# Performance work log

Measured on AMD Instinct MI355X. Metric: run time of the kernel, lower is better.

## Reference

```python
import jax, jax.numpy as jnp
import numpy as np

N_NODES = 50000
N_EDGES = 600000
CH = 128      # units / channels
RBF = 200     # ceil(cutoff/gap) = ceil(20.0/0.1)
LOG2 = 0.6931471805599453


def shifted_softplus(x):
    # tf.where(x < 14, softplus(where(x < 14, x, 0)), x) - log(2)
    safe = jnp.where(x < 14.0, x, jnp.zeros_like(x))
    return jnp.where(x < 14.0, jax.nn.softplus(safe), x) - LOG2


def _glorot(key, shape):
    fan_in = shape[0] if len(shape) > 1 else shape[0]
    fan_out = shape[-1]
    lim = np.sqrt(6.0 / (fan_in + fan_out))
    return jax.random.uniform(key, shape, jnp.float32, -lim, lim)


def setup_inputs() -> dict:
    key = jax.random.key(0)
    ks = jax.random.split(key, 12)
    rbf = jax.random.uniform(ks[0], (N_EDGES, RBF), jnp.float32)
    x = jax.random.normal(ks[1], (N_NODES, CH), jnp.float32)
    src = jax.random.randint(ks[2], (N_EDGES,), 0, N_NODES, jnp.int32)
    return {
        "rbf": rbf,
        "x": x,
        "src": src,
        "w1": _glorot(ks[3], (RBF, CH)),
        "b1": _glorot(ks[4], (CH,)),
        "w2": _glorot(ks[5], (CH, CH)),
        "b2": _glorot(ks[6], (CH,)),
        "w3": _glorot(ks[7], (CH, CH)),
        "w4": _glorot(ks[8], (CH, CH)),
        "b4": _glorot(ks[9], (CH,)),
        "w5": _glorot(ks[10], (CH, CH)),
        "b5": _glorot(ks[11], (CH,)),
    }


def reference(rbf, x, src, w1, b1, w2, b2, w3, w4, b4, w5, b5):
    # filter-generating MLP on edge RBF features: [E, RBF] -> [E, CH]
    h = shifted_softplus(rbf @ w1 + b1)
    w = shifted_softplus(h @ w2 + b2)
    # node feature transform, gather to edges by SOURCE index
    f = x @ w3                         # [N, CH]
    wf = w * f[src]                    # [E, CH] broadcast_node_to_edges + multiply
    # scatter-sum edges back to SOURCE nodes
    conv = jax.ops.segment_sum(wf, src, num_segments=N_NODES)  # [N, CH]
    # output MLP + residual
    y = shifted_softplus(conv @ w4 + b4)
    v = y @ w5 + b5
    return x + v
```

## Files before the change

kernel.cpp:

```cpp
#include <hip/hip_runtime.h>

#define CH      128
#define RBFD    200
#define NNODES  50000
#define NEDGES  600000
#define LOG2F_  0.6931471805599453f

#define W1F_ELEMS (8 * 7 * 64 * 8)
#define W2F_ELEMS (8 * 4 * 64 * 8)
#define WF_TOT    (W1F_ELEMS + W2F_ELEMS)

typedef __attribute__((ext_vector_type(8))) __bf16 bf16x8;
typedef __attribute__((ext_vector_type(4))) float  f32x4;

__device__ __forceinline__ float ssp(float x) {
    float e  = __expf(x);
    float sp = __logf(1.0f + e);
    sp = (x < 14.0f) ? sp : x;
    return sp - LOG2F_;
}

__device__ __forceinline__ unsigned short f2bf(float f) {
    union { float f; unsigned int u; } v; v.f = f;
    unsigned int r = v.u + 0x7FFFu + ((v.u >> 16) & 1u);
    return (unsigned short)(r >> 16);
}

__device__ __forceinline__ float bf2f(unsigned short s) {
    union { unsigned int u; float f; } v; v.u = ((unsigned int)s) << 16;
    return v.f;
}

__device__ __forceinline__ unsigned short cvt1bf(float f) {
    unsigned int u;
    asm("v_cvt_pk_bf16_f32 %0, %1, %2" : "=v"(u) : "v"(f), "v"(f));
    return (unsigned short)u;
}

__device__ __forceinline__ bf16x8 load_cvt8(const float* p) {
    float4 f0 = *(const float4*)p;
    float4 f1 = *(const float4*)(p + 4);
    union { unsigned int u[4]; bf16x8 v; } r;
    asm("v_cvt_pk_bf16_f32 %0, %1, %2" : "=v"(r.u[0]) : "v"(f0.x), "v"(f0.y));
    asm("v_cvt_pk_bf16_f32 %0, %1, %2" : "=v"(r.u[1]) : "v"(f0.z), "v"(f0.w));
    asm("v_cvt_pk_bf16_f32 %0, %1, %2" : "=v"(r.u[2]) : "v"(f1.x), "v"(f1.y));
    asm("v_cvt_pk_bf16_f32 %0, %1, %2" : "=v"(r.u[3]) : "v"(f1.z), "v"(f1.w));
    return r.v;
}

__global__ __launch_bounds__(256) void prep_weights_frag(const float* __restrict__ w1,
                                                         const float* __restrict__ w2,
                                                         unsigned short* __restrict__ w1F,
                                                         unsigned short* __restrict__ w2F) {
    int i = blockIdx.x * 256 + threadIdx.x;
    if (i < W1F_ELEMS) {
        int frag = i >> 9;
        int lane = (i >> 3) & 63;
        int j    = i & 7;
        int nt = frag / 7, kt = frag % 7;
        int n = nt * 16 + (lane & 15);
        int k = kt * 32 + (lane >> 4) * 8 + j;
        w1F[i] = (k < RBFD) ? f2bf(w1[k * CH + n]) : (unsigned short)0;
    } else if (i < WF_TOT) {
        int q = i - W1F_ELEMS;
        int frag = q >> 9;
        int lane = (q >> 3) & 63;
        int j    = q & 7;
        int nt = frag >> 2, kt = frag & 3;
        int n = nt * 16 + (lane & 15);
        int k = kt * 32 + (lane >> 4) * 8 + j;
        w2F[q] = f2bf(w2[k * CH + n]);
    }
}

__global__ __launch_bounds__(256) void k_hist(const int* __restrict__ src, int* __restrict__ cur) {
    int e = blockIdx.x * 256 + threadIdx.x;
    if (e < NEDGES) atomicAdd(&cur[src[e]], 1);
}

__global__ __launch_bounds__(256) void k_scan1(const int* __restrict__ cur, int* __restrict__ bsum) {
    __shared__ int s[256];
    const int t = threadIdx.x;
    int i = blockIdx.x * 256 + t;
    s[t] = (i < NNODES) ? cur[i] : 0;
    __syncthreads();
    for (int d = 128; d > 0; d >>= 1) {
        if (t < d) s[t] += s[t + d];
        __syncthreads();
    }
    if (t == 0) bsum[blockIdx.x] = s[0];
}

__global__ __launch_bounds__(256) void k_scan2(const int* __restrict__ bsum, int* __restrict__ bpre) {
    __shared__ int s[256];
    const int t = threadIdx.x;
    int v0 = (t < 196) ? bsum[t] : 0;
    s[t] = v0;
    __syncthreads();
    for (int d = 1; d < 256; d <<= 1) {
        int v = (t >= d) ? s[t - d] : 0;
        __syncthreads();
        s[t] += v;
        __syncthreads();
    }
    if (t < 196) bpre[t] = s[t] - v0;
}

__global__ __launch_bounds__(256) void k_scan3(const int* __restrict__ deg_in,
                                               const int* __restrict__ bpre,
                                               int* __restrict__ csr_off,
                                               int* __restrict__ cur) {
    __shared__ int s[256];
    const int t = threadIdx.x, b = blockIdx.x;
    const int i = b * 256 + t;
    int d0 = (i < NNODES) ? deg_in[i] : 0;
    s[t] = d0;
    __syncthreads();
    for (int d = 1; d < 256; d <<= 1) {
        int v = (t >= d) ? s[t - d] : 0;
        __syncthreads();
        s[t] += v;
        __syncthreads();
    }
    if (i < NNODES) {
        int ex = bpre[b] + s[t] - d0;
        csr_off[i] = ex;
        cur[i] = ex;
    }
    if (i == NNODES - 1) csr_off[NNODES] = NEDGES;
}

__global__ __launch_bounds__(256) void k_fill(const int* __restrict__ src,
                                              int* __restrict__ cur,
                                              int* __restrict__ eidx) {
    int e = blockIdx.x * 256 + threadIdx.x;
    if (e < NEDGES) {
        int pos = atomicAdd(&cur[src[e]], 1);
        eidx[pos] = e;
    }
}

__global__ __launch_bounds__(256, 8) void edge_kernel4(const float* __restrict__ rbf,
                                                       const float* __restrict__ b1v,
                                                       const float* __restrict__ b2v,
                                                       const unsigned short* __restrict__ w1F,
                                                       const unsigned short* __restrict__ w2F,
                                                       unsigned short* __restrict__ wbuf) {
    __shared__ unsigned short tile[4][16 * 128];
    const int t = threadIdx.x;
    const int lane = t & 63;
    const int wv = t >> 6;
    const int l15 = lane & 15;
    const int lg  = lane >> 4;
    const size_t erow0 = (size_t)blockIdx.x * 64 + (size_t)wv * 16;
    char* myb = (char*)(tile[wv]);

    const bf16x8* w1v = (const bf16x8*)w1F;
    const bf16x8* w2v = (const bf16x8*)w2F;

    bf16x8 a1[7];
    const float* arow = rbf + (erow0 + l15) * RBFD;
#pragma unroll
    for (int kt = 0; kt < 6; kt++)
        a1[kt] = load_cvt8(arow + kt * 32 + lg * 8);
    if (lg == 0) {
        a1[6] = load_cvt8(arow + 192);
    } else {
        union { unsigned int u[4]; bf16x8 v; } z;
        z.u[0] = z.u[1] = z.u[2] = z.u[3] = 0;
        a1[6] = z.v;
    }

    const int myrow0 = lg * 4;

#pragma unroll
    for (int nt = 0; nt < 8; nt++) {
        f32x4 acc = {0.f, 0.f, 0.f, 0.f};
#pragma unroll
        for (int kt = 0; kt < 7; kt++) {
            bf16x8 b = w1v[((nt * 7 + kt) << 6) + lane];
            acc = __builtin_amdgcn_mfma_f32_16x16x32_bf16(a1[kt], b, acc, 0, 0, 0);
        }
        const float bias = b1v[nt * 16 + l15];
#pragma unroll
        for (int r = 0; r < 4; r++) {
            const int row = myrow0 + r;
            const int colb = (nt * 32 + l15 * 2) ^ ((row & 7) << 4);
            *(unsigned short*)(myb + row * 256 + colb) = cvt1bf(ssp(acc[r] + bias));
        }
    }

    bf16x8 a2[4];
#pragma unroll
    for (int kt = 0; kt < 4; kt++) {
        const int boff = l15 * 256 + ((kt * 64 + lg * 16) ^ ((l15 & 7) << 4));
        a2[kt] = *(const bf16x8*)(myb + boff);
    }

#pragma unroll
    for (int nt = 0; nt < 8; nt++) {
        f32x4 acc = {0.f, 0.f, 0.f, 0.f};
#pragma unroll
        for (int kt = 0; kt < 4; kt++) {
            bf16x8 b = w2v[((nt * 4 + kt) << 6) + lane];
            acc = __builtin_amdgcn_mfma_f32_16x16x32_bf16(a2[kt], b, acc, 0, 0, 0);
        }
        const float bias = b2v[nt * 16 + l15];
#pragma unroll
        for (int r = 0; r < 4; r++) {
            const int row = myrow0 + r;
            const int colb = (nt * 32 + l15 * 2) ^ ((row & 7) << 4);
            *(unsigned short*)(myb + row * 256 + colb) = cvt1bf(ssp(acc[r] + bias));
        }
    }

    {
        const int row = lane >> 2, q = lane & 3;
        float4 o[4];
#pragma unroll
        for (int j = 0; j < 4; j++) {
            const int boff = row * 256 + ((q * 64 + j * 16) ^ ((row & 7) << 4));
            o[j] = *(const float4*)(myb + boff);
        }
        float4* gdst = (float4*)((char*)wbuf + (erow0 + row) * 256 + q * 64);
#pragma unroll
        for (int j = 0; j < 4; j++) gdst[j] = o[j];
    }
}

__global__ __launch_bounds__(256) void node_gather2(const float* __restrict__ x,
                                                    const float* __restrict__ w3,
                                                    const float* __restrict__ w4,
                                                    const float* __restrict__ b4,
                                                    const float* __restrict__ w5,
                                                    const float* __restrict__ b5,
                                                    const unsigned short* __restrict__ wbuf,
                                                    const int* __restrict__ eidx,
                                                    const int* __restrict__ csr_off,
                                                    float* __restrict__ out,
                                                    int n_nodes) {
    __shared__ float A[32 * 128];
    __shared__ float B[32 * 128];
    const int t = threadIdx.x;
    const int n0 = blockIdx.x * 32;
    const int rows = min(32, n_nodes - n0);

    {
        const float4* g = (const float4*)(x + (size_t)n0 * CH);
        float4* s = (float4*)A;
        for (int i = t; i < rows * 32; i += 256) s[i] = g[i];
    }
    __syncthreads();

    const int c = t & 127, eh = t >> 7;
    float acc[16];

#pragma unroll
    for (int i = 0; i < 16; i++) acc[i] = 0.f;
    for (int k = 0; k < 128; k += 4) {
        const float wa = w3[(k + 0) * CH + c];
        const float wb = w3[(k + 1) * CH + c];
        const float wc = w3[(k + 2) * CH + c];
        const float wd = w3[(k + 3) * CH + c];
#pragma unroll
        for (int i = 0; i < 16; i++) {
            const float4 v = *(const float4*)&A[(eh * 16 + i) * CH + k];
            acc[i] = fmaf(v.x, wa, acc[i]);
            acc[i] = fmaf(v.y, wb, acc[i]);
            acc[i] = fmaf(v.z, wc, acc[i]);
            acc[i] = fmaf(v.w, wd, acc[i]);
        }
    }
#pragma unroll
    for (int i = 0; i < 16; i++) B[(eh * 16 + i) * 128 + c] = acc[i];
    __syncthreads();

    {
        const int lane = t & 63, wv = t >> 6;
        const int c0 = lane * 2;
        for (int rr = 0; rr < 8; rr++) {
            const int r = wv * 8 + rr;
            const int n = n0 + r;
            float s0 = 0.f, s1 = 0.f;
            if (n < n_nodes) {
                const int o0 = csr_off[n], o1 = csr_off[n + 1];
                int j = o0;
                for (; j + 3 < o1; j += 4) {
                    const int ea = eidx[j], eb = eidx[j + 1], ec = eidx[j + 2], ed = eidx[j + 3];
                    const unsigned ua = *(const unsigned*)(wbuf + (size_t)ea * CH + c0);
                    const unsigned ub = *(const unsigned*)(wbuf + (size_t)eb * CH + c0);
                    const unsigned uc = *(const unsigned*)(wbuf + (size_t)ec * CH + c0);
                    const unsigned ud = *(const unsigned*)(wbuf + (size_t)ed * CH + c0);
                    s0 += bf2f((unsigned short)ua) + bf2f((unsigned short)ub)
                        + bf2f((unsigned short)uc) + bf2f((unsigned short)ud);
                    s1 += bf2f((unsigned short)(ua >> 16)) + bf2f((unsigned short)(ub >> 16))
                        + bf2f((unsigned short)(uc >> 16)) + bf2f((unsigned short)(ud >> 16));
                }
                for (; j < o1; j++) {
                    const unsigned ua = *(const unsigned*)(wbuf + (size_t)eidx[j] * CH + c0);
                    s0 += bf2f((unsigned short)ua);
                    s1 += bf2f((unsigned short)(ua >> 16));
                }
            }
            const float2 f2 = *(const float2*)&B[r * 128 + c0];
            float2 v2;
            v2.x = (n < n_nodes) ? f2.x * s0 : 0.f;
            v2.y = (n < n_nodes) ? f2.y * s1 : 0.f;
            *(float2*)&B[r * 128 + c0] = v2;
        }
    }
    __syncthreads();

#pragma unroll
    for (int i = 0; i < 16; i++) acc[i] = 0.f;
    for (int k = 0; k < 128; k += 4) {
        const float wa = w4[(k + 0) * CH + c];
        const float wb = w4[(k + 1) * CH + c];
        const float wc = w4[(k + 2) * CH + c];
        const float wd = w4[(k + 3) * CH + c];
#pragma unroll
        for (int i = 0; i < 16; i++) {
            const float4 v = *(const float4*)&B[(eh * 16 + i) * CH + k];
            acc[i] = fmaf(v.x, wa, acc[i]);
            acc[i] = fmaf(v.y, wb, acc[i]);
            acc[i] = fmaf(v.z, wc, acc[i]);
            acc[i] = fmaf(v.w, wd, acc[i]);
        }
    }
    {
        const float bias4 = b4[c];
#pragma unroll
        for (int i = 0; i < 16; i++)
            A[(eh * 16 + i) * 128 + c] = ssp(acc[i] + bias4);
    }
    __syncthreads();

#pragma unroll
    for (int i = 0; i < 16; i++) acc[i] = 0.f;
    for (int k = 0; k < 128; k += 4) {
        const float wa = w5[(k + 0) * CH + c];
        const float wb = w5[(k + 1) * CH + c];
        const float wc = w5[(k + 2) * CH + c];
        const float wd = w5[(k + 3) * CH + c];
#pragma unroll
        for (int i = 0; i < 16; i++) {
            const float4 v = *(const float4*)&A[(eh * 16 + i) * CH + k];
            acc[i] = fmaf(v.x, wa, acc[i]);
            acc[i] = fmaf(v.y, wb, acc[i]);
            acc[i] = fmaf(v.z, wc, acc[i]);
            acc[i] = fmaf(v.w, wd, acc[i]);
        }
    }
    {
        const float bias5 = b5[c];
#pragma unroll
        for (int i = 0; i < 16; i++) {
            const int r = eh * 16 + i;
            if (r < rows) {
                const size_t off = ((size_t)(n0 + r)) * CH + c;
                out[off] = x[off] + acc[i] + bias5;
            }
        }
    }
}

static inline size_t align_up(size_t v, size_t a) { return (v + a - 1) & ~(a - 1); }

extern "C" void kernel_launch(void* const* d_in, const int* in_sizes, int n_in,
                              void* d_out, int out_size, void* d_ws, size_t ws_size,
                              hipStream_t stream) {
    const float* rbf = (const float*)d_in[0];
    const float* x   = (const float*)d_in[1];
    const int*   src = (const int*)d_in[2];
    const float* w1  = (const float*)d_in[3];
    const float* b1  = (const float*)d_in[4];
    const float* w2  = (const float*)d_in[5];
    const float* b2  = (const float*)d_in[6];
    const float* w3  = (const float*)d_in[7];
    const float* w4  = (const float*)d_in[8];
    const float* b4  = (const float*)d_in[9];
    const float* w5  = (const float*)d_in[10];
    const float* b5  = (const float*)d_in[11];

    float* out = (float*)d_out;

    size_t off = 0;
    const size_t o_wbuf = off;  off = align_up(off + (size_t)NEDGES * CH * 2, 256);
    const size_t o_eidx = off;  off = align_up(off + (size_t)NEDGES * 4, 256);
    const size_t o_csr  = off;  off = align_up(off + (size_t)(NNODES + 1) * 4, 256);
    const size_t o_cur  = off;  off = align_up(off + (size_t)NNODES * 4, 256);
    const size_t o_bs   = off;  off = align_up(off + 256 * 4, 256);
    const size_t o_bp   = off;  off = align_up(off + 256 * 4, 256);
    const size_t o_wF   = off;  off = align_up(off + (size_t)WF_TOT * 2, 256);

    unsigned short* wbuf = (unsigned short*)((char*)d_ws + o_wbuf);
    int* eidx            = (int*)((char*)d_ws + o_eidx);
    int* csr_off         = (int*)((char*)d_ws + o_csr);
    int* cur             = (int*)((char*)d_ws + o_cur);
    int* bsum            = (int*)((char*)d_ws + o_bs);
    int* bpre            = (int*)((char*)d_ws + o_bp);
    unsigned short* w1F  = (unsigned short*)((char*)d_ws + o_wF);
    unsigned short* w2F  = w1F + W1F_ELEMS;

    hipMemsetAsync(cur, 0, (size_t)NNODES * 4, stream);
    prep_weights_frag<<<(WF_TOT + 255) / 256, 256, 0, stream>>>(w1, w2, w1F, w2F);
    edge_kernel4<<<NEDGES / 64, 256, 0, stream>>>(rbf, b1, b2, w1F, w2F, wbuf);
    k_hist<<<(NEDGES + 255) / 256, 256, 0, stream>>>(src, cur);
    k_scan1<<<196, 256, 0, stream>>>(cur, bsum);
    k_scan2<<<1, 256, 0, stream>>>(bsum, bpre);
    k_scan3<<<196, 256, 0, stream>>>(cur, bpre, csr_off, cur);
    k_fill<<<(NEDGES + 255) / 256, 256, 0, stream>>>(src, cur, eidx);
    node_gather2<<<(NNODES + 31) / 32, 256, 0, stream>>>(x, w3, w4, b4, w5, b5,
                                                         wbuf, eidx, csr_off, out, NNODES);
}
```

Measured before the change: 565.1 us.

## Stage RBF tile in LDS and split output columns across waves in edge MLP

The edge MLP kernel now handles 32 edges per block. It loads the RBF rows cooperatively with coalesced float4 reads, converts them to bf16 and stores them in padded shared memory. Each wave then computes two 16-column output tiles for all 32 rows, instead of one wave computing all columns for its own 16 rows. This cuts per-wave weight fragment loads and improves coalescing of the rbf read, at the cost of block-wide barriers and more LDS traffic. The launch-bounds occupancy hint is removed.

Measured after the change: 492.1 us. 1.15x faster.

```diff
diff --git a/kernel.cpp b/kernel.cpp
--- a/kernel.cpp
+++ b/kernel.cpp
@@ -5,6 +5,8 @@
 #define NNODES  50000
 #define NEDGES  600000
 #define LOG2F_  0.6931471805599453f
+#define RSTR    232
+#define HSTR    136
 
 #define W1F_ELEMS (8 * 7 * 64 * 8)
 #define W2F_ELEMS (8 * 4 * 64 * 8)
@@ -37,15 +39,10 @@
     return (unsigned short)u;
 }
 
-__device__ __forceinline__ bf16x8 load_cvt8(const float* p) {
-    float4 f0 = *(const float4*)p;
-    float4 f1 = *(const float4*)(p + 4);
-    union { unsigned int u[4]; bf16x8 v; } r;
-    asm("v_cvt_pk_bf16_f32 %0, %1, %2" : "=v"(r.u[0]) : "v"(f0.x), "v"(f0.y));
-    asm("v_cvt_pk_bf16_f32 %0, %1, %2" : "=v"(r.u[1]) : "v"(f0.z), "v"(f0.w));
-    asm("v_cvt_pk_bf16_f32 %0, %1, %2" : "=v"(r.u[2]) : "v"(f1.x), "v"(f1.y));
-    asm("v_cvt_pk_bf16_f32 %0, %1, %2" : "=v"(r.u[3]) : "v"(f1.z), "v"(f1.w));
-    return r.v;
+__device__ __forceinline__ unsigned int cvt2bf(float lo, float hi) {
+    unsigned int u;
+    asm("v_cvt_pk_bf16_f32 %0, %1, %2" : "=v"(u) : "v"(lo), "v"(hi));
+    return u;
 }
 
 __global__ __launch_bounds__(256) void prep_weights_frag(const float* __restrict__ w1,
@@ -140,91 +137,95 @@
     }
 }
 
-__global__ __launch_bounds__(256, 8) void edge_kernel4(const float* __restrict__ rbf,
-                                                       const float* __restrict__ b1v,
-                                                       const float* __restrict__ b2v,
-                                                       const unsigned short* __restrict__ w1F,
-                                                       const unsigned short* __restrict__ w2F,
-                                                       unsigned short* __restrict__ wbuf) {
-    __shared__ unsigned short tile[4][16 * 128];
+__global__ __launch_bounds__(256) void edge_kernel7(const float* __restrict__ rbf,
+                                                    const float* __restrict__ b1v,
+                                                    const float* __restrict__ b2v,
+                                                    const unsigned short* __restrict__ w1F,
+                                                    const unsigned short* __restrict__ w2F,
+                                                    unsigned short* __restrict__ wbuf) {
+    __shared__ unsigned short rbf_s[32 * RSTR];
+    __shared__ unsigned short h_s[32 * HSTR];
+    unsigned short* w_s = rbf_s;
     const int t = threadIdx.x;
     const int lane = t & 63;
     const int wv = t >> 6;
     const int l15 = lane & 15;
     const int lg  = lane >> 4;
-    const size_t erow0 = (size_t)blockIdx.x * 64 + (size_t)wv * 16;
-    char* myb = (char*)(tile[wv]);
+    const size_t e0 = (size_t)blockIdx.x * 32;
 
     const bf16x8* w1v = (const bf16x8*)w1F;
     const bf16x8* w2v = (const bf16x8*)w2F;
 
-    bf16x8 a1[7];
-    const float* arow = rbf + (erow0 + l15) * RBFD;
-#pragma unroll
-    for (int kt = 0; kt < 6; kt++)
-        a1[kt] = load_cvt8(arow + kt * 32 + lg * 8);
-    if (lg == 0) {
-        a1[6] = load_cvt8(arow + 192);
-    } else {
-        union { unsigned int u[4]; bf16x8 v; } z;
-        z.u[0] = z.u[1] = z.u[2] = z.u[3] = 0;
-        a1[6] = z.v;
-    }
-
+    {
+        const float4* g = (const float4*)(rbf + e0 * RBFD);
+        for (int i = t; i < 1600; i += 256) {
+            float4 v = g[i];
+            int row = i / 50, c4 = (i % 50) * 4;
+            union { unsigned int u[2]; unsigned long long ull; } p;
+            p.u[0] = cvt2bf(v.x, v.y);
+            p.u[1] = cvt2bf(v.z, v.w);
+            *(unsigned long long*)&rbf_s[row * RSTR + c4] = p.ull;
+        }
+        for (int i = t; i < 768; i += 256) {
+            int row = i / 24, k = RBFD + (i % 24);
+            rbf_s[row * RSTR + k] = 0;
+        }
+    }
+    __syncthreads();
+
+    const float bias10 = b1v[wv * 32 + l15];
+    const float bias11 = b1v[wv * 32 + 16 + l15];
     const int myrow0 = lg * 4;
 
 #pragma unroll
-    for (int nt = 0; nt < 8; nt++) {
-        f32x4 acc = {0.f, 0.f, 0.f, 0.f};
+    for (int m = 0; m < 2; m++) {
+        f32x4 acc0 = {0.f, 0.f, 0.f, 0.f};
+        f32x4 acc1 = {0.f, 0.f, 0.f, 0.f};
+        const unsigned short* abase = &rbf_s[(m * 16 + l15) * RSTR + lg * 8];
+        const int nt0 = wv * 2, nt1 = wv * 2 + 1;
 #pragma unroll
         for (int kt = 0; kt < 7; kt++) {
-            bf16x8 b = w1v[((nt * 7 + kt) << 6) + lane];
-            acc = __builtin_amdgcn_mfma_f32_16x16x32_bf16(a1[kt], b, acc, 0, 0, 0);
-        }
-        const float bias = b1v[nt * 16 + l15];
+            bf16x8 a = *(const bf16x8*)(abase + kt * 32);
+            acc0 = __builtin_amdgcn_mfma_f32_16x16x32_bf16(a, w1v[((nt0 * 7 + kt) << 6) + lane], acc0, 0, 0, 0);
+            acc1 = __builtin_amdgcn_mfma_f32_16x16x32_bf16(a, w1v[((nt1 * 7 + kt) << 6) + lane], acc1, 0, 0, 0);
+        }
+        const int hrow0 = m * 16 + myrow0;
 #pragma unroll
         for (int r = 0; r < 4; r++) {
-            const int row = myrow0 + r;
-            const int colb = (nt * 32 + l15 * 2) ^ ((row & 7) << 4);
-            *(unsigned short*)(myb + row * 256 + colb) = cvt1bf(ssp(acc[r] + bias));
-        }
-    }
-
-    bf16x8 a2[4];
-#pragma unroll
-    for (int kt = 0; kt < 4; kt++) {
-        const int boff = l15 * 256 + ((kt * 64 + lg * 16) ^ ((l15 & 7) << 4));
-        a2[kt] = *(const bf16x8*)(myb + boff);
-    }
-
-#pragma unroll
-    for (int nt = 0; nt < 8; nt++) {
-        f32x4 acc = {0.f, 0.f, 0.f, 0.f};
+            h_s[(hrow0 + r) * HSTR + wv * 32 + l15]      = cvt1bf(ssp(acc0[r] + bias10));
+            h_s[(hrow0 + r) * HSTR + wv * 32 + 16 + l15] = cvt1bf(ssp(acc1[r] + bias11));
+        }
+    }
+    __syncthreads();
+
+    const float bias20 = b2v[wv * 32 + l15];
+    const float bias21 = b2v[wv * 32 + 16 + l15];
+
+#pragma unroll
+    for (int m = 0; m < 2; m++) {
+        f32x4 acc0 = {0.f, 0.f, 0.f, 0.f};
+        f32x4 acc1 = {0.f, 0.f, 0.f, 0.f};
+        const unsigned short* abase = &h_s[(m * 16 + l15) * HSTR + lg * 8];
+        const int nt0 = wv * 2, nt1 = wv * 2 + 1;
 #pragma unroll
         for (int kt = 0; kt < 4; kt++) {
-            bf16x8 b = w2v[((nt * 4 + kt) << 6) + lane];
-            acc = __builtin_amdgcn_mfma_f32_16x16x32_bf16(a2[kt], b, acc, 0, 0, 0);
-        }
-        const float bias = b2v[nt * 16 + l15];
+            bf16x8 a = *(const bf16x8*)(abase + kt * 32);
+            acc0 = __builtin_amdgcn_mfma_f32_16x16x32_bf16(a, w2v[((nt0 * 4 + kt) << 6) + lane], acc0, 0, 0, 0);
+            acc1 = __builtin_amdgcn_mfma_f32_16x16x32_bf16(a, w2v[((nt1 * 4 + kt) << 6) + lane], acc1, 0, 0, 0);
+        }
+        const int wrow0 = m * 16 + myrow0;
 #pragma unroll
         for (int r = 0; r < 4; r++) {
-            const int row = myrow0 + r;
-            const int colb = (nt * 32 + l15 * 2) ^ ((row & 7) << 4);
-            *(unsigned short*)(myb + row * 256 + colb) = cvt1bf(ssp(acc[r] + bias));
-        }
-    }
-
-    {
-        const int row = lane >> 2, q = lane & 3;
-        float4 o[4];
-#pragma unroll
-        for (int j = 0; j < 4; j++) {
-            const int boff = row * 256 + ((q * 64 + j * 16) ^ ((row & 7) << 4));
-            o[j] = *(const float4*)(myb + boff);
-        }
-        float4* gdst = (float4*)((char*)wbuf + (erow0 + row) * 256 + q * 64);
-#pragma unroll
-        for (int j = 0; j < 4; j++) gdst[j] = o[j];
+            w_s[(wrow0 + r) * HSTR + wv * 32 + l15]      = cvt1bf(ssp(acc0[r] + bias20));
+            w_s[(wrow0 + r) * HSTR + wv * 32 + 16 + l15] = cvt1bf(ssp(acc1[r] + bias21));
+        }
+    }
+    __syncthreads();
+
+    for (int i = t; i < 512; i += 256) {
+        const int row = i >> 4, q = i & 15;
+        float4 v = *(const float4*)&w_s[row * HSTR + q * 8];
+        ((float4*)wbuf)[(e0 + row) * 16 + q] = v;
     }
 }
 
@@ -404,7 +405,7 @@
 
     hipMemsetAsync(cur, 0, (size_t)NNODES * 4, stream);
     prep_weights_frag<<<(WF_TOT + 255) / 256, 256, 0, stream>>>(w1, w2, w1F, w2F);
-    edge_kernel4<<<NEDGES / 64, 256, 0, stream>>>(rbf, b1, b2, w1F, w2F, wbuf);
+    edge_kernel7<<<NEDGES / 32, 256, 0, stream>>>(rbf, b1, b2, w1F, w2F, wbuf);
     k_hist<<<(NEDGES + 255) / 256, 256, 0, stream>>>(src, cur);
     k_scan1<<<196, 256, 0, stream>>>(cur, bsum);
     k_scan2<<<1, 256, 0, stream>>>(bsum, bpre);
```
